# Optimization experiments

Hardware: AMD Instinct MI355X
Metric: run time of the kernel (lower is better)

Reference implementation:

```python
import jax, jax.numpy as jnp
import numpy as np

B, S, D, H = 128, 1024, 256, 256


def setup_inputs() -> dict:
    key = jax.random.key(0)
    k1, k2, k3 = jax.random.split(key, 3)
    x = jax.random.normal(k1, (B, S, D), dtype=jnp.float32)
    mask = jnp.ones((B, S), dtype=jnp.float32)
    # GRU params (torch.nn.GRUCell convention, gate order r, z, n), scaled init
    sc = 1.0 / np.sqrt(H)
    W_ih = jax.random.normal(k2, (D, 3 * H), dtype=jnp.float32) * sc
    W_hh = jax.random.normal(k3, (H, 3 * H), dtype=jnp.float32) * sc
    b_ih = jnp.zeros((3 * H,), dtype=jnp.float32)
    b_hh = jnp.zeros((3 * H,), dtype=jnp.float32)
    return {"x": x, "mask": mask, "W_ih": W_ih, "W_hh": W_hh, "b_ih": b_ih, "b_hh": b_hh}


def _gru_scan(x, mask, W_ih, W_hh, b_ih, b_hh):
    # x: [B,S,D], mask: [B,S] -> outputs [B,S,H] (return_all=True, reverse=False)
    Hd = W_hh.shape[0]
    h0 = jnp.zeros((x.shape[0], Hd), dtype=x.dtype)
    xs = jnp.swapaxes(x, 0, 1)            # [S,B,D]
    ms = jnp.swapaxes(mask, 0, 1)[..., None]  # [S,B,1]

    def step(h, inp):
        x_t, m_t = inp
        gx = x_t @ W_ih + b_ih            # [B,3H]
        gh = h @ W_hh + b_hh              # [B,3H]
        gx_r, gx_z, gx_n = jnp.split(gx, 3, axis=-1)
        gh_r, gh_z, gh_n = jnp.split(gh, 3, axis=-1)
        r = jax.nn.sigmoid(gx_r + gh_r)
        z = jax.nn.sigmoid(gx_z + gh_z)
        n = jnp.tanh(gx_n + r * gh_n)
        h_new = (1.0 - z) * n + z * h
        h = m_t * h_new + (1.0 - m_t) * h  # mask_t gating per cell(x_t, mask_t)
        return h, h

    _, ys = jax.lax.scan(step, h0, (xs, ms))  # ys: [S,B,H]
    return jnp.swapaxes(ys, 0, 1)             # [B,S,H]


def reference(x, mask, W_ih, W_hh, b_ih, b_hh):
    return _gru_scan(x, mask, W_ih, W_hh, b_ih, b_hh)
```

## Files before the change

### kernel.cpp

```cpp
#include <hip/hip_runtime.h>

typedef _Float16 f16;
typedef _Float16 half2t __attribute__((ext_vector_type(2)));
typedef _Float16 half8 __attribute__((ext_vector_type(8)));
typedef float floatx4 __attribute__((ext_vector_type(4)));

#define B_ 128
#define S_ 1024
#define D_ 256
#define H_ 256
#define N3H 768

__global__ void pack_whh_kernel(const float* __restrict__ whh,
                                unsigned int* __restrict__ whh2) {
  int idx = blockIdx.x * 256 + threadIdx.x;
  if (idx >= 128 * N3H) return;
  int k2 = idx / N3H;
  int j  = idx - k2 * N3H;
  f16 lo = (f16)whh[(2 * k2) * N3H + j];
  f16 hi = (f16)whh[(2 * k2 + 1) * N3H + j];
  unsigned int v = ((unsigned int)__builtin_bit_cast(unsigned short, lo)) |
                   ((unsigned int)__builtin_bit_cast(unsigned short, hi) << 16);
  whh2[idx] = v;
}

__global__ __launch_bounds__(256) void gemm_gx_kernel(
    const float* __restrict__ X, const float* __restrict__ W,
    const float* __restrict__ bias, f16* __restrict__ gx) {
  __shared__ __align__(16) f16 As[128][40];
  __shared__ __align__(16) f16 Bs[128][40];
  const int m0 = blockIdx.x * 128;
  const int n0 = blockIdx.y * 128;
  const int tid = threadIdx.x;
  const int lane = tid & 63, wave = tid >> 6;
  const int wr = (wave >> 1) * 64, wc = (wave & 1) * 64;
  const int quad = lane >> 4, l16 = lane & 15;

  floatx4 acc[4][4];
#pragma unroll
  for (int i = 0; i < 4; i++)
#pragma unroll
    for (int j = 0; j < 4; j++) acc[i][j] = (floatx4)0.f;

  const int arow = tid >> 1, akh = (tid & 1) * 16;
  const int bkr = tid >> 3, bns = (tid & 7) * 16;

  for (int k0 = 0; k0 < 256; k0 += 32) {
    __syncthreads();
    {
      const float* src = X + (size_t)(m0 + arow) * 256 + k0 + akh;
      float4 f0 = ((const float4*)src)[0];
      float4 f1 = ((const float4*)src)[1];
      float4 f2 = ((const float4*)src)[2];
      float4 f3 = ((const float4*)src)[3];
      half8 v0 = {(f16)f0.x, (f16)f0.y, (f16)f0.z, (f16)f0.w,
                  (f16)f1.x, (f16)f1.y, (f16)f1.z, (f16)f1.w};
      half8 v1 = {(f16)f2.x, (f16)f2.y, (f16)f2.z, (f16)f2.w,
                  (f16)f3.x, (f16)f3.y, (f16)f3.z, (f16)f3.w};
      *(half8*)&As[arow][akh] = v0;
      *(half8*)&As[arow][akh + 8] = v1;
    }
    {
      const float* src = W + (size_t)(k0 + bkr) * N3H + n0 + bns;
      float4 f0 = ((const float4*)src)[0];
      float4 f1 = ((const float4*)src)[1];
      float4 f2 = ((const float4*)src)[2];
      float4 f3 = ((const float4*)src)[3];
      float fv[16] = {f0.x, f0.y, f0.z, f0.w, f1.x, f1.y, f1.z, f1.w,
                      f2.x, f2.y, f2.z, f2.w, f3.x, f3.y, f3.z, f3.w};
#pragma unroll
      for (int i = 0; i < 16; ++i) Bs[bns + i][bkr] = (f16)fv[i];
    }
    __syncthreads();
    half8 a[4], b[4];
#pragma unroll
    for (int i = 0; i < 4; ++i) a[i] = *(const half8*)&As[wr + i * 16 + l16][quad * 8];
#pragma unroll
    for (int j = 0; j < 4; ++j) b[j] = *(const half8*)&Bs[wc + j * 16 + l16][quad * 8];
#pragma unroll
    for (int i = 0; i < 4; ++i)
#pragma unroll
      for (int j = 0; j < 4; ++j)
        acc[i][j] = __builtin_amdgcn_mfma_f32_16x16x32_f16(a[i], b[j], acc[i][j], 0, 0, 0);
  }
#pragma unroll
  for (int i = 0; i < 4; ++i) {
#pragma unroll
    for (int j = 0; j < 4; ++j) {
      int col = n0 + wc + j * 16 + l16;
      float bv = bias[col];
#pragma unroll
      for (int r = 0; r < 4; ++r) {
        int row = m0 + wr + i * 16 + quad * 4 + r;
        gx[(size_t)row * N3H + col] = (f16)(acc[i][j][r] + bv);
      }
    }
  }
}

__global__ __launch_bounds__(768) void gru_rec_kernel(
    const f16* __restrict__ gx,
    const unsigned int* __restrict__ w2,
    const float* __restrict__ bhh,
    const float* __restrict__ mask,
    float* __restrict__ out) {
  const int b = blockIdx.x;
  const int j = threadIdx.x;
  __shared__ __align__(16) f16 h16[256];
  __shared__ float rz[512];

  unsigned int w[128];
#pragma unroll
  for (int k2 = 0; k2 < 128; ++k2) w[k2] = w2[k2 * N3H + j];

  if (j < 256) h16[j] = (f16)0.f;
  const float bj = bhh[j];
  const f16* gxp = gx + (size_t)b * S_ * N3H + j;
  const float* mp = mask + (size_t)b * S_;
  float* outp = out + (size_t)b * S_ * H_;

  __syncthreads();

  f16 cur_gx = gxp[0];
  float cur_m = mp[0];
  for (int t = 0; t < S_; ++t) {
    f16 nxt_gx = (f16)0.f;
    float nxt_m = 0.f;
    if (t + 1 < S_) {
      nxt_gx = gxp[(size_t)(t + 1) * N3H];
      nxt_m = mp[t + 1];
    }
    float acc = 0.f;
    const uint4* h4 = (const uint4*)h16;
#pragma unroll
    for (int c = 0; c < 32; ++c) {
      uint4 hc = h4[c];
      acc = __builtin_amdgcn_fdot2(__builtin_bit_cast(half2t, hc.x),
                                   __builtin_bit_cast(half2t, w[c * 4 + 0]), acc, false);
      acc = __builtin_amdgcn_fdot2(__builtin_bit_cast(half2t, hc.y),
                                   __builtin_bit_cast(half2t, w[c * 4 + 1]), acc, false);
      acc = __builtin_amdgcn_fdot2(__builtin_bit_cast(half2t, hc.z),
                                   __builtin_bit_cast(half2t, w[c * 4 + 2]), acc, false);
      acc = __builtin_amdgcn_fdot2(__builtin_bit_cast(half2t, hc.w),
                                   __builtin_bit_cast(half2t, w[c * 4 + 3]), acc, false);
    }
    float gh = acc + bj;
    float gxv = (float)cur_gx;
    if (j < 512) {
      float xa = gxv + gh;
      xa = fminf(fmaxf(xa, -30.f), 30.f);
      rz[j] = 1.f / (1.f + __expf(-xa));
    }
    __syncthreads();
    if (j >= 512) {
      const int jj = j - 512;
      float r = rz[jj], z = rz[jj + 256];
      float xn = gxv + r * gh;
      xn = fminf(fmaxf(xn, -15.f), 15.f);
      float e = __expf(2.f * xn);
      float n = (e - 1.f) / (e + 1.f);
      float hp = (float)h16[jj];
      float hn = (1.f - z) * n + z * hp;
      float hv = cur_m * hn + (1.f - cur_m) * hp;
      h16[jj] = (f16)hv;
      outp[(size_t)t * H_ + jj] = hv;
    }
    __syncthreads();
    cur_gx = nxt_gx;
    cur_m = nxt_m;
  }
}

extern "C" void kernel_launch(void* const* d_in, const int* in_sizes, int n_in,
                              void* d_out, int out_size, void* d_ws, size_t ws_size,
                              hipStream_t stream) {
  const float* x    = (const float*)d_in[0];
  const float* mask = (const float*)d_in[1];
  const float* Wih  = (const float*)d_in[2];
  const float* Whh  = (const float*)d_in[3];
  const float* bih  = (const float*)d_in[4];
  const float* bhh  = (const float*)d_in[5];
  float* out = (float*)d_out;

  f16* gx = (f16*)d_ws;
  unsigned int* whh2 =
      (unsigned int*)((char*)d_ws + (size_t)B_ * S_ * N3H * sizeof(f16));

  pack_whh_kernel<<<dim3((128 * N3H + 255) / 256), dim3(256), 0, stream>>>(Whh, whh2);
  gemm_gx_kernel<<<dim3((B_ * S_) / 128, N3H / 128), dim3(256), 0, stream>>>(x, Wih, bih, gx);
  gru_rec_kernel<<<dim3(B_), dim3(768), 0, stream>>>(gx, whh2, bhh, mask, out);
}
```

Baseline: 1.628 ms.

## Compute all three gates per thread in GRU recurrence with double-buffered hidden state

The recurrent kernel drops from 768 threads (one gate column each) to 256 threads, each computing the r, z and n dot products for one hidden unit. This removes the shared rz exchange and one of the two block barriers per timestep. The hidden state is double-buffered in shared memory so a single barrier per step is enough. In exchange each thread now holds 384 packed weight registers, which risks spilling or AGPR shuffling, and there is only one wave per SIMD to hide latency.

Measured after the change: 2.953 ms. 1.81x slower.

```diff
diff --git a/kernel.cpp b/kernel.cpp
--- a/kernel.cpp
+++ b/kernel.cpp
@@ -98,7 +98,7 @@
   }
 }
 
-__global__ __launch_bounds__(768) void gru_rec_kernel(
+__global__ __launch_bounds__(256, 1) void gru_rec_kernel(
     const f16* __restrict__ gx,
     const unsigned int* __restrict__ w2,
     const float* __restrict__ bhh,
@@ -106,68 +106,90 @@
     float* __restrict__ out) {
   const int b = blockIdx.x;
   const int j = threadIdx.x;
-  __shared__ __align__(16) f16 h16[256];
-  __shared__ float rz[512];
-
-  unsigned int w[128];
-#pragma unroll
-  for (int k2 = 0; k2 < 128; ++k2) w[k2] = w2[k2 * N3H + j];
-
-  if (j < 256) h16[j] = (f16)0.f;
-  const float bj = bhh[j];
+  __shared__ __align__(16) f16 h16[2][256];
+
+  unsigned int wr[128], wz[128], wn[128];
+#pragma unroll
+  for (int c = 0; c < 128; ++c) wr[c] = w2[c * N3H + j];
+#pragma unroll
+  for (int c = 0; c < 128; ++c) wz[c] = w2[c * N3H + j + 256];
+#pragma unroll
+  for (int c = 0; c < 128; ++c) wn[c] = w2[c * N3H + j + 512];
+
+  const float br = bhh[j];
+  const float bz = bhh[j + 256];
+  const float bn = bhh[j + 512];
   const f16* gxp = gx + (size_t)b * S_ * N3H + j;
   const float* mp = mask + (size_t)b * S_;
-  float* outp = out + (size_t)b * S_ * H_;
-
+  float* outp = out + (size_t)b * S_ * H_ + j;
+
+  h16[0][j] = (f16)0.f;
   __syncthreads();
 
-  f16 cur_gx = gxp[0];
-  float cur_m = mp[0];
+  f16 gxr = gxp[0], gxz = gxp[256], gxn = gxp[512];
+  float m = mp[0];
+
   for (int t = 0; t < S_; ++t) {
-    f16 nxt_gx = (f16)0.f;
-    float nxt_m = 0.f;
+    f16 ngxr = (f16)0.f, ngxz = (f16)0.f, ngxn = (f16)0.f;
+    float nm = 0.f;
     if (t + 1 < S_) {
-      nxt_gx = gxp[(size_t)(t + 1) * N3H];
-      nxt_m = mp[t + 1];
-    }
-    float acc = 0.f;
-    const uint4* h4 = (const uint4*)h16;
+      const f16* np = gxp + (size_t)(t + 1) * N3H;
+      ngxr = np[0];
+      ngxz = np[256];
+      ngxn = np[512];
+      nm = mp[t + 1];
+    }
+
+    const uint4* h4 = (const uint4*)&h16[t & 1][0];
+    float ar = 0.f, az = 0.f, an = 0.f;
 #pragma unroll
     for (int c = 0; c < 32; ++c) {
       uint4 hc = h4[c];
-      acc = __builtin_amdgcn_fdot2(__builtin_bit_cast(half2t, hc.x),
-                                   __builtin_bit_cast(half2t, w[c * 4 + 0]), acc, false);
-      acc = __builtin_amdgcn_fdot2(__builtin_bit_cast(half2t, hc.y),
-                                   __builtin_bit_cast(half2t, w[c * 4 + 1]), acc, false);
-      acc = __builtin_amdgcn_fdot2(__builtin_bit_cast(half2t, hc.z),
-                                   __builtin_bit_cast(half2t, w[c * 4 + 2]), acc, false);
-      acc = __builtin_amdgcn_fdot2(__builtin_bit_cast(half2t, hc.w),
-                                   __builtin_bit_cast(half2t, w[c * 4 + 3]), acc, false);
-    }
-    float gh = acc + bj;
-    float gxv = (float)cur_gx;
-    if (j < 512) {
-      float xa = gxv + gh;
-      xa = fminf(fmaxf(xa, -30.f), 30.f);
-      rz[j] = 1.f / (1.f + __expf(-xa));
-    }
+      half2t h0 = __builtin_bit_cast(half2t, hc.x);
+      half2t h1 = __builtin_bit_cast(half2t, hc.y);
+      half2t h2 = __builtin_bit_cast(half2t, hc.z);
+      half2t h3 = __builtin_bit_cast(half2t, hc.w);
+      ar = __builtin_amdgcn_fdot2(h0, __builtin_bit_cast(half2t, wr[c * 4 + 0]), ar, false);
+      az = __builtin_amdgcn_fdot2(h0, __builtin_bit_cast(half2t, wz[c * 4 + 0]), az, false);
+      an = __builtin_amdgcn_fdot2(h0, __builtin_bit_cast(half2t, wn[c * 4 + 0]), an, false);
+      ar = __builtin_amdgcn_fdot2(h1, __builtin_bit_cast(half2t, wr[c * 4 + 1]), ar, false);
+      az = __builtin_amdgcn_fdot2(h1, __builtin_bit_cast(half2t, wz[c * 4 + 1]), az, false);
+      an = __builtin_amdgcn_fdot2(h1, __builtin_bit_cast(half2t, wn[c * 4 + 1]), an, false);
+      ar = __builtin_amdgcn_fdot2(h2, __builtin_bit_cast(half2t, wr[c * 4 + 2]), ar, false);
+      az = __builtin_amdgcn_fdot2(h2, __builtin_bit_cast(half2t, wz[c * 4 + 2]), az, false);
+      an = __builtin_amdgcn_fdot2(h2, __builtin_bit_cast(half2t, wn[c * 4 + 2]), an, false);
+      ar = __builtin_amdgcn_fdot2(h3, __builtin_bit_cast(half2t, wr[c * 4 + 3]), ar, false);
+      az = __builtin_amdgcn_fdot2(h3, __builtin_bit_cast(half2t, wz[c * 4 + 3]), az, false);
+      an = __builtin_amdgcn_fdot2(h3, __builtin_bit_cast(half2t, wn[c * 4 + 3]), an, false);
+    }
+
+    float ghr = ar + br;
+    float ghz = az + bz;
+    float ghn = an + bn;
+    float xr = (float)gxr + ghr;
+    float xz = (float)gxz + ghz;
+    xr = fminf(fmaxf(xr, -30.f), 30.f);
+    xz = fminf(fmaxf(xz, -30.f), 30.f);
+    float r = 1.f / (1.f + __expf(-xr));
+    float z = 1.f / (1.f + __expf(-xz));
+    float xn = (float)gxn + r * ghn;
+    xn = fminf(fmaxf(xn, -15.f), 15.f);
+    float e = __expf(2.f * xn);
+    float n = (e - 1.f) / (e + 1.f);
+
+    float hp = (float)h16[t & 1][j];
+    float hnew = (1.f - z) * n + z * hp;
+    float hv = m * hnew + (1.f - m) * hp;
+
+    h16[(t + 1) & 1][j] = (f16)hv;
+    outp[(size_t)t * H_] = hv;
+
     __syncthreads();
-    if (j >= 512) {
-      const int jj = j - 512;
-      float r = rz[jj], z = rz[jj + 256];
-      float xn = gxv + r * gh;
-      xn = fminf(fmaxf(xn, -15.f), 15.f);
-      float e = __expf(2.f * xn);
-      float n = (e - 1.f) / (e + 1.f);
-      float hp = (float)h16[jj];
-      float hn = (1.f - z) * n + z * hp;
-      float hv = cur_m * hn + (1.f - cur_m) * hp;
-      h16[jj] = (f16)hv;
-      outp[(size_t)t * H_ + jj] = hv;
-    }
-    __syncthreads();
-    cur_gx = nxt_gx;
-    cur_m = nxt_m;
+
+    gxr = ngxr;
+    gxz = ngxz;
+    gxn = ngxn;
+    m = nm;
   }
 }
 
@@ -188,5 +210,5 @@
 
   pack_whh_kernel<<<dim3((128 * N3H + 255) / 256), dim3(256), 0, stream>>>(Whh, whh2);
   gemm_gx_kernel<<<dim3((B_ * S_) / 128, N3H / 128), dim3(256), 0, stream>>>(x, Wih, bih, gx);
-  gru_rec_kernel<<<dim3(B_), dim3(768), 0, stream>>>(gx, whh2, bhh, mask, out);
-}
+  gru_rec_kernel<<<dim3(B_), dim3(256), 0, stream>>>(gx, whh2, bhh, mask, out);
+}
```
